# Kernel optimization log

Hardware: AMD Instinct MI355X
Metric: run time of the kernel (lower is better)

Reference implementation:

```python
import jax, jax.numpy as jnp
import numpy as np

FEATS = 1024
HEAD = 16
MLP_HIDDEN = 4096
HEAD_DIM = FEATS // HEAD
SQRT_D = float(FEATS) ** 0.5  # module scales by sqrt(feats), not sqrt(head_dim)
LN_EPS = 1e-5


def layer_norm(x, g, b):
    mu = jnp.mean(x, axis=-1, keepdims=True)
    var = jnp.mean(jnp.square(x - mu), axis=-1, keepdims=True)
    return (x - mu) * jax.lax.rsqrt(var + LN_EPS) * g + b


def setup_inputs() -> dict:
    key = jax.random.key(0)
    ks = jax.random.split(key, 12)
    s = 1.0 / np.sqrt(FEATS)
    s2 = 1.0 / np.sqrt(MLP_HIDDEN)
    return {
        "x": jax.random.normal(ks[0], (2, 2048, FEATS), dtype=jnp.float32),
        "ln1_g": jnp.ones((FEATS,), jnp.float32),
        "ln1_b": jnp.zeros((FEATS,), jnp.float32),
        "wq": jax.random.normal(ks[1], (FEATS, FEATS), jnp.float32) * s,
        "bq": jnp.zeros((FEATS,), jnp.float32),
        "wk": jax.random.normal(ks[2], (FEATS, FEATS), jnp.float32) * s,
        "bk": jnp.zeros((FEATS,), jnp.float32),
        "wv": jax.random.normal(ks[3], (FEATS, FEATS), jnp.float32) * s,
        "bv": jnp.zeros((FEATS,), jnp.float32),
        "wo": jax.random.normal(ks[4], (FEATS, FEATS), jnp.float32) * s,
        "bo": jnp.zeros((FEATS,), jnp.float32),
        "ln2_g": jnp.ones((FEATS,), jnp.float32),
        "ln2_b": jnp.zeros((FEATS,), jnp.float32),
        "w1": jax.random.normal(ks[5], (MLP_HIDDEN, FEATS), jnp.float32) * s,
        "b1": jnp.zeros((MLP_HIDDEN,), jnp.float32),
        "w2": jax.random.normal(ks[6], (FEATS, MLP_HIDDEN), jnp.float32) * s2,
        "b2": jnp.zeros((FEATS,), jnp.float32),
    }


def reference(x, ln1_g, ln1_b, wq, bq, wk, bk, wv, bv, wo, bo,
              ln2_g, ln2_b, w1, b1, w2, b2):
    b, n, f = x.shape
    h = layer_norm(x, ln1_g, ln1_b)
    # qkv projections (torch Linear: y = x @ W.T + b)
    q = (h @ wq.T + bq).reshape(b, n, HEAD, HEAD_DIM).transpose(0, 2, 1, 3)
    k = (h @ wk.T + bk).reshape(b, n, HEAD, HEAD_DIM).transpose(0, 2, 1, 3)
    v = (h @ wv.T + bv).reshape(b, n, HEAD, HEAD_DIM).transpose(0, 2, 1, 3)
    score = jax.nn.softmax(jnp.einsum('bhif,bhjf->bhij', q, k) / SQRT_D, axis=-1)
    attn = jnp.einsum('bhij,bhjf->bihf', score, v).reshape(b, n, f)
    o = attn @ wo.T + bo
    out1 = o + x
    h2 = layer_norm(out1, ln2_g, ln2_b)
    mlp = jax.nn.relu(jax.nn.relu(h2 @ w1.T + b1) @ w2.T + b2)
    return mlp + out1
```

## Files before the change

kernel.cpp:

```cpp
#include <hip/hip_runtime.h>
#include <hip/hip_bf16.h>

#define FEATS 1024
#define NH 16
#define HD 64
#define SEQ 2048
#define BATCH 2
#define MTOT (BATCH*SEQ)
#define MLPH 4096
#define QSCALE 0.04508422277369218f

typedef __attribute__((ext_vector_type(8))) short bf16x8;
typedef __attribute__((ext_vector_type(4))) short bf16x4;
typedef __attribute__((ext_vector_type(4))) float f32x4;

static_assert(sizeof(bf16x8) == 16, "bf16x8 must be 16B");

__device__ __forceinline__ unsigned short f2bf(float f) {
    unsigned int u = __float_as_uint(f);
    unsigned int lsb = (u >> 16) & 1u;
    u += 0x7fffu + lsb;
    return (unsigned short)(u >> 16);
}

#define ASYNC16(GP, LP) __builtin_amdgcn_global_load_lds( \
    (const __attribute__((address_space(1))) void*)(GP),  \
    (__attribute__((address_space(3))) void*)(LP), 16, 0, 0)

__global__ __launch_bounds__(256) void cvt_all_kernel(
    const float* __restrict__ wq, const float* __restrict__ wk,
    const float* __restrict__ wv, const float* __restrict__ wo,
    const float* __restrict__ w1, const float* __restrict__ w2,
    unsigned short* __restrict__ dst) {
    const size_t i = ((size_t)blockIdx.x * 256 + threadIdx.x) * 4;
    const size_t MB = (size_t)1024 * 1024;
    const float* s;
    size_t off;
    float sc = 1.0f;
    if (i < MB)            { s = wq; off = i;          sc = QSCALE; }
    else if (i < 2 * MB)   { s = wk; off = i - MB; }
    else if (i < 3 * MB)   { s = wv; off = i - 2 * MB; }
    else if (i < 4 * MB)   { s = wo; off = i - 3 * MB; }
    else if (i < 8 * MB)   { s = w1; off = i - 4 * MB; }
    else                   { s = w2; off = i - 8 * MB; }
    float4 v = *(const float4*)(s + off);
    ushort4 o;
    o.x = f2bf(v.x * sc); o.y = f2bf(v.y * sc);
    o.z = f2bf(v.z * sc); o.w = f2bf(v.w * sc);
    *(ushort4*)(dst + i) = o;
}

__global__ __launch_bounds__(256) void concat3_kernel(const float* __restrict__ a,
                                                      const float* __restrict__ b,
                                                      const float* __restrict__ c,
                                                      float* __restrict__ o) {
    int i = blockIdx.x * 256 + threadIdx.x;
    float v = (i < 1024) ? a[i] * QSCALE : ((i < 2048) ? b[i - 1024] : c[i - 2048]);
    o[i] = v;
}

__global__ __launch_bounds__(256) void ln_kernel(const float* __restrict__ x,
                                                 const float* __restrict__ g,
                                                 const float* __restrict__ bta,
                                                 unsigned short* __restrict__ h) {
    __shared__ float red[8];
    const int row = blockIdx.x;
    const int t = threadIdx.x;
    const float* xr = x + (size_t)row * FEATS;
    float4 v = ((const float4*)xr)[t];
    float s  = v.x + v.y + v.z + v.w;
    float ss = v.x * v.x + v.y * v.y + v.z * v.z + v.w * v.w;
#pragma unroll
    for (int off = 1; off < 64; off <<= 1) {
        s  += __shfl_xor(s, off);
        ss += __shfl_xor(ss, off);
    }
    const int w = t >> 6;
    if ((t & 63) == 0) { red[w] = s; red[4 + w] = ss; }
    __syncthreads();
    s  = red[0] + red[1] + red[2] + red[3];
    ss = red[4] + red[5] + red[6] + red[7];
    const float mu  = s * (1.f / FEATS);
    const float var = ss * (1.f / FEATS) - mu * mu;
    const float rs  = rsqrtf(var + 1e-5f);
    float4 gv = ((const float4*)g)[t];
    float4 bv = ((const float4*)bta)[t];
    ushort4 ov;
    ov.x = f2bf((v.x - mu) * rs * gv.x + bv.x);
    ov.y = f2bf((v.y - mu) * rs * gv.y + bv.y);
    ov.z = f2bf((v.z - mu) * rs * gv.z + bv.z);
    ov.w = f2bf((v.w - mu) * rs * gv.w + bv.w);
    ((ushort4*)h)[(size_t)row * (FEATS / 4) + t] = ov;
}

template <bool RELU, bool ADD, bool OUTBF16>
__global__ __launch_bounds__(256, 3)
void gemm_kernel(const unsigned short* __restrict__ A,
                 const unsigned short* __restrict__ W,
                 const float* __restrict__ bias,
                 const float* __restrict__ addend,
                 void* __restrict__ outp,
                 int M, int N, int K, int gx) {
    __shared__ unsigned short lds[3][2][128 * 32];

    const int t = threadIdx.x;
    const int w = t >> 6, lane = t & 63;
    const int wr = w >> 1, wc = w & 1;
    const int li = lane & 15, lj = lane >> 4;

    const int nwg = gridDim.x;
    const int cpx = nwg >> 3;
    const int wg = blockIdx.x;
    const int swz = (wg & 7) * cpx + (wg >> 3);
    const int mb = (swz / gx) * 128, nb = (swz % gx) * 128;

    const int srow = lane >> 2;
    const int scg = ((lane & 3) ^ (srow & 3)) * 8;
    const unsigned short* gA = A + (size_t)(mb + w * 16 + srow) * K + scg;
    const unsigned short* gB = W + (size_t)(nb + w * 16 + srow) * K + scg;
    const size_t half = (size_t)64 * K;
    const int lbase = w * 512 + lane * 8;

    const int rsw = (lj ^ (li & 3)) * 8;

    const int nt = K >> 5;

#define STAGE(BUF, K0)                                             \
    do {                                                           \
        unsigned short* la_ = &lds[BUF][0][lbase];                 \
        unsigned short* lb_ = &lds[BUF][1][lbase];                 \
        ASYNC16(gA + (K0), la_);                                   \
        ASYNC16(gA + half + (K0), la_ + 2048);                     \
        ASYNC16(gB + (K0), lb_);                                   \
        ASYNC16(gB + half + (K0), lb_ + 2048);                     \
    } while (0)

    STAGE(0, 0);
    STAGE(1, 32);
    asm volatile("s_waitcnt vmcnt(4)" ::: "memory");
    __builtin_amdgcn_s_barrier();

    f32x4 acc[4][4] = {};

    for (int i = 0; i < nt; ++i) {
        const int cur = i % 3;
        const unsigned short* Al = &lds[cur][0][0];
        const unsigned short* Bl = &lds[cur][1][0];

        bf16x8 af[4], bfr[4];
#pragma unroll
        for (int m = 0; m < 4; m++)
            af[m] = *(const bf16x8*)(Al + (wr * 64 + m * 16 + li) * 32 + rsw);
#pragma unroll
        for (int n = 0; n < 4; n++)
            bfr[n] = *(const bf16x8*)(Bl + (wc * 64 + n * 16 + li) * 32 + rsw);

        const int pf = i + 2 < nt;
        if (pf) STAGE((i + 2) % 3, (i + 2) * 32);

#pragma unroll
        for (int m = 0; m < 4; m++)
#pragma unroll
            for (int n = 0; n < 4; n++)
                acc[m][n] = __builtin_amdgcn_mfma_f32_16x16x32_bf16(af[m], bfr[n], acc[m][n], 0, 0, 0);

        if (i + 1 < nt) {
            if (pf) asm volatile("s_waitcnt vmcnt(4)" ::: "memory");
            else    asm volatile("s_waitcnt vmcnt(0)" ::: "memory");
            __builtin_amdgcn_s_barrier();
        }
    }
#undef STAGE

#pragma unroll
    for (int m = 0; m < 4; m++) {
#pragma unroll
        for (int n = 0; n < 4; n++) {
            const int col = nb + wc * 64 + n * 16 + li;
            const float bv = bias[col];
#pragma unroll
            for (int r = 0; r < 4; r++) {
                const int row = mb + wr * 64 + m * 16 + lj * 4 + r;
                float v = acc[m][n][r] + bv;
                if (RELU) v = fmaxf(v, 0.f);
                if (ADD)  v += addend[(size_t)row * N + col];
                if (OUTBF16)
                    ((unsigned short*)outp)[(size_t)row * N + col] = f2bf(v);
                else
                    ((float*)outp)[(size_t)row * N + col] = v;
            }
        }
    }
}

__global__ __launch_bounds__(256) void vtrans_kernel(const unsigned short* __restrict__ qkv,
                                                     unsigned short* __restrict__ vt) {
    constexpr int LDV = 68;
    __shared__ unsigned short Vl[64 * LDV];
    const int bh = blockIdx.x, st = blockIdx.y;
    const int b = bh >> 4, h = bh & 15;
    const int t = threadIdx.x;
    const unsigned short* src = qkv + (size_t)(b * SEQ + st * 64) * (3 * FEATS) + 2 * FEATS + h * HD;
#pragma unroll
    for (int i = 0; i < 2; i++) {
        int idx = t + i * 256;
        int r = idx >> 3, c = (idx & 7) * 8;
        *(bf16x8*)(Vl + r * LDV + c) = *(const bf16x8*)(src + (size_t)r * (3 * FEATS) + c);
    }
    __syncthreads();
    unsigned short* dst = vt + (size_t)bh * HD * SEQ + st * 64;
#pragma unroll
    for (int i = 0; i < 2; i++) {
        int idx = t + i * 256;
        int d = idx >> 3, s8 = (idx & 7) * 8;
        const int base = s8 & ~31;
        const int u4 = ((s8 >> 3) & 3) * 4;
        bf16x8 v;
#pragma unroll
        for (int j = 0; j < 8; j++) {
            const int key = base + u4 + (j & 3) + ((j >> 2) & 1) * 16;
            v[j] = Vl[key * LDV + d];
        }
        *(bf16x8*)(dst + (size_t)d * SEQ + s8) = v;
    }
}

__global__ __launch_bounds__(256, 4)
void attn_kernel(const unsigned short* __restrict__ qkv,
                 const unsigned short* __restrict__ vt,
                 unsigned short* __restrict__ out) {
    constexpr int LK = 72;
    __shared__ unsigned short Kl[2][64 * LK];
    __shared__ unsigned short Vtl[2][64 * LK];

    const int bh = blockIdx.x;
    const int b = bh >> 4, h = bh & 15;
    const int q0 = blockIdx.y * 128;
    const int t = threadIdx.x, w = t >> 6, lane = t & 63;
    const int li = lane & 15, lj = lane >> 4;

    const size_t rstr = 3 * FEATS;
    const unsigned short* qkvb = qkv + (size_t)(b * SEQ) * rstr;
    const unsigned short* ksrc = qkvb + FEATS + h * HD;
    const unsigned short* vsrc = vt + (size_t)bh * HD * SEQ;

    bf16x8 aq[2][2];
#pragma unroll
    for (int hh = 0; hh < 2; hh++)
#pragma unroll
        for (int kk = 0; kk < 2; kk++)
            aq[hh][kk] = *(const bf16x8*)(qkvb +
                (size_t)(q0 + w * 32 + hh * 16 + li) * rstr + h * HD + kk * 32 + lj * 8);

    f32x4 o[2][4] = {};
    f32x4 oS[2] = {};

    const short onebf = (short)0x3F80;
    const bf16x8 ones = {onebf, onebf, onebf, onebf, onebf, onebf, onebf, onebf};

    const int sr = t >> 2, sc = (t & 3) * 16;
    const unsigned short* kg = ksrc + (size_t)sr * rstr + sc;
    const unsigned short* vg = vsrc + (size_t)sr * SEQ + sc;
    const int ldo = sr * LK + sc;

    const int nt = SEQ / 64;

    {
        bf16x8 k0 = *(const bf16x8*)kg;
        bf16x8 k1 = *(const bf16x8*)(kg + 8);
        bf16x8 v0 = *(const bf16x8*)vg;
        bf16x8 v1 = *(const bf16x8*)(vg + 8);
        *(bf16x8*)(&Kl[0][ldo])      = k0;
        *(bf16x8*)(&Kl[0][ldo + 8])  = k1;
        *(bf16x8*)(&Vtl[0][ldo])     = v0;
        *(bf16x8*)(&Vtl[0][ldo + 8]) = v1;
    }

    int cur = 0;
    for (int i = 0; i < nt; ++i) {
        bf16x8 kr0, kr1, vr0, vr1;
        if (i + 1 < nt) {
            const unsigned short* kn = kg + (size_t)(i + 1) * 64 * rstr;
            const unsigned short* vn = vg + (i + 1) * 64;
            kr0 = *(const bf16x8*)kn;
            kr1 = *(const bf16x8*)(kn + 8);
            vr0 = *(const bf16x8*)vn;
            vr1 = *(const bf16x8*)(vn + 8);
        }

        asm volatile("s_waitcnt lgkmcnt(0)" ::: "memory");
        __builtin_amdgcn_s_barrier();

        const unsigned short* Kc = Kl[cur];
        const unsigned short* Vc = Vtl[cur];

        f32x4 s[2][4];
        __builtin_amdgcn_s_setprio(1);
#pragma unroll
        for (int n = 0; n < 4; n++) {
            bf16x8 k0 = *(const bf16x8*)(Kc + (n * 16 + li) * LK + lj * 8);
            bf16x8 k1 = *(const bf16x8*)(Kc + (n * 16 + li) * LK + 32 + lj * 8);
#pragma unroll
            for (int hh = 0; hh < 2; hh++) {
                f32x4 acc = {};
                acc = __builtin_amdgcn_mfma_f32_16x16x32_bf16(k0, aq[hh][0], acc, 0, 0, 0);
                acc = __builtin_amdgcn_mfma_f32_16x16x32_bf16(k1, aq[hh][1], acc, 0, 0, 0);
                s[hh][n] = acc;
            }
        }
        __builtin_amdgcn_s_setprio(0);

        bf16x8 A[2][2];
#pragma unroll
        for (int hh = 0; hh < 2; hh++)
#pragma unroll
            for (int kk = 0; kk < 2; kk++) {
                float p[8];
#pragma unroll
                for (int r = 0; r < 4; r++) {
                    p[r]     = exp2f(s[hh][2 * kk][r]);
                    p[4 + r] = exp2f(s[hh][2 * kk + 1][r]);
                }
                union { unsigned u[4]; bf16x8 v; } Au;
                asm("v_cvt_pk_bf16_f32 %0, %1, %2" : "=v"(Au.u[0]) : "v"(p[0]), "v"(p[1]));
                asm("v_cvt_pk_bf16_f32 %0, %1, %2" : "=v"(Au.u[1]) : "v"(p[2]), "v"(p[3]));
                asm("v_cvt_pk_bf16_f32 %0, %1, %2" : "=v"(Au.u[2]) : "v"(p[4]), "v"(p[5]));
                asm("v_cvt_pk_bf16_f32 %0, %1, %2" : "=v"(Au.u[3]) : "v"(p[6]), "v"(p[7]));
                A[hh][kk] = Au.v;
            }

#pragma unroll
        for (int hh = 0; hh < 2; hh++)
#pragma unroll
            for (int kk = 0; kk < 2; kk++)
                oS[hh] = __builtin_amdgcn_mfma_f32_16x16x32_bf16(A[hh][kk], ones, oS[hh], 0, 0, 0);

        __builtin_amdgcn_s_setprio(1);
#pragma unroll
        for (int n = 0; n < 4; n++) {
#pragma unroll
            for (int kk = 0; kk < 2; kk++) {
                bf16x8 bv = *(const bf16x8*)(Vc + (n * 16 + li) * LK + kk * 32 + lj * 8);
                o[0][n] = __builtin_amdgcn_mfma_f32_16x16x32_bf16(A[0][kk], bv, o[0][n], 0, 0, 0);
                o[1][n] = __builtin_amdgcn_mfma_f32_16x16x32_bf16(A[1][kk], bv, o[1][n], 0, 0, 0);
            }
        }
        __builtin_amdgcn_s_setprio(0);

        if (i + 1 < nt) {
            *(bf16x8*)(&Kl[cur ^ 1][ldo])      = kr0;
            *(bf16x8*)(&Kl[cur ^ 1][ldo + 8])  = kr1;
            *(bf16x8*)(&Vtl[cur ^ 1][ldo])     = vr0;
            *(bf16x8*)(&Vtl[cur ^ 1][ldo + 8]) = vr1;
        }
        cur ^= 1;
    }

    unsigned short* ob = out + (size_t)(b * SEQ + q0 + w * 32) * FEATS + h * HD;
#pragma unroll
    for (int hh = 0; hh < 2; hh++)
#pragma unroll
        for (int r = 0; r < 4; r++) {
            const float inv = 1.f / oS[hh][r];
#pragma unroll
            for (int n = 0; n < 4; n++)
                ob[(size_t)(hh * 16 + lj * 4 + r) * FEATS + n * 16 + li] =
                    f2bf(o[hh][n][r] * inv);
        }
}

extern "C" void kernel_launch(void* const* d_in, const int* in_sizes, int n_in,
                              void* d_out, int out_size, void* d_ws, size_t ws_size,
                              hipStream_t stream) {
    const float* x     = (const float*)d_in[0];
    const float* ln1_g = (const float*)d_in[1];
    const float* ln1_b = (const float*)d_in[2];
    const float* wq    = (const float*)d_in[3];
    const float* bq    = (const float*)d_in[4];
    const float* wk    = (const float*)d_in[5];
    const float* bk    = (const float*)d_in[6];
    const float* wv    = (const float*)d_in[7];
    const float* bvv   = (const float*)d_in[8];
    const float* wo    = (const float*)d_in[9];
    const float* bo    = (const float*)d_in[10];
    const float* ln2_g = (const float*)d_in[11];
    const float* ln2_b = (const float*)d_in[12];
    const float* w1    = (const float*)d_in[13];
    const float* b1    = (const float*)d_in[14];
    const float* w2    = (const float*)d_in[15];
    const float* b2    = (const float*)d_in[16];

    unsigned short* wqkv_b = (unsigned short*)d_ws;
    unsigned short* wo_b   = wqkv_b + 3072 * 1024;
    unsigned short* w1_b   = wo_b + 1024 * 1024;
    unsigned short* w2_b   = w1_b + 4096 * 1024;
    float*          bqkv   = (float*)(w2_b + 1024 * 4096);
    unsigned short* region = (unsigned short*)(bqkv + 3072);
    unsigned short* qkvb   = region;
    unsigned short* hb     = region + (size_t)4096 * 3072;
    unsigned short* vtb    = hb;
    unsigned short* a1     = region;
    unsigned short* attn_o = region + (size_t)4096 * 4096;
    unsigned short* h2     = attn_o;
    float*          out1   = (float*)(attn_o + (size_t)4096 * 1024);
    float*          outf   = (float*)d_out;

    dim3 blk(256);

    cvt_all_kernel<<<12288, blk, 0, stream>>>(wq, wk, wv, wo, w1, w2, wqkv_b);
    concat3_kernel<<<12, blk, 0, stream>>>(bq, bk, bvv, bqkv);

    ln_kernel<<<MTOT, blk, 0, stream>>>(x, ln1_g, ln1_b, hb);

    gemm_kernel<false, false, true><<<768, blk, 0, stream>>>(
        hb, wqkv_b, bqkv, nullptr, qkvb, MTOT, 3072, FEATS, 24);

    vtrans_kernel<<<dim3(BATCH * NH, SEQ / 64), blk, 0, stream>>>(qkvb, vtb);

    attn_kernel<<<dim3(BATCH * NH, SEQ / 128), dim3(256), 0, stream>>>(qkvb, vtb, attn_o);

    gemm_kernel<false, true, false><<<256, blk, 0, stream>>>(
        attn_o, wo_b, bo, x, out1, MTOT, FEATS, FEATS, 8);

    ln_kernel<<<MTOT, blk, 0, stream>>>(out1, ln2_g, ln2_b, h2);

    gemm_kernel<true, false, true><<<1024, blk, 0, stream>>>(
        h2, w1_b, b1, nullptr, a1, MTOT, MLPH, FEATS, 32);

    gemm_kernel<true, true, false><<<256, blk, 0, stream>>>(
        a1, w2_b, b2, out1, outf, MTOT, FEATS, MLPH, 8);
}
```

Before: 233.3 us.

## Split attention over two KV halves and combine partial results

Adds a grid z-dimension so each attention block processes half of the key sequence, writing unnormalized bf16 partial outputs and row denominators to a scratch buffer. A new combine kernel sums the two partials and normalizes. This doubles the number of attention blocks to fill more CUs, at the cost of extra global traffic, an additional launch, and rounding unnormalized partials to bf16.

```diff
diff --git a/kernel.cpp b/kernel.cpp
--- a/kernel.cpp
+++ b/kernel.cpp
@@ -228,7 +228,8 @@
 __global__ __launch_bounds__(256, 4)
 void attn_kernel(const unsigned short* __restrict__ qkv,
                  const unsigned short* __restrict__ vt,
-                 unsigned short* __restrict__ out) {
+                 unsigned short* __restrict__ nbuf,
+                 float* __restrict__ den) {
     constexpr int LK = 72;
     __shared__ unsigned short Kl[2][64 * LK];
     __shared__ unsigned short Vtl[2][64 * LK];
@@ -236,6 +237,7 @@
     const int bh = blockIdx.x;
     const int b = bh >> 4, h = bh & 15;
     const int q0 = blockIdx.y * 128;
+    const int sp = blockIdx.z;
     const int t = threadIdx.x, w = t >> 6, lane = t & 63;
     const int li = lane & 15, lj = lane >> 4;
 
@@ -259,11 +261,11 @@
     const bf16x8 ones = {onebf, onebf, onebf, onebf, onebf, onebf, onebf, onebf};
 
     const int sr = t >> 2, sc = (t & 3) * 16;
-    const unsigned short* kg = ksrc + (size_t)sr * rstr + sc;
-    const unsigned short* vg = vsrc + (size_t)sr * SEQ + sc;
+    const unsigned short* kg = ksrc + (size_t)(sp * 1024 + sr) * rstr + sc;
+    const unsigned short* vg = vsrc + (size_t)sr * SEQ + sp * 1024 + sc;
     const int ldo = sr * LK + sc;
 
-    const int nt = SEQ / 64;
+    const int nt = 1024 / 64;
 
     {
         bf16x8 k0 = *(const bf16x8*)kg;
@@ -356,17 +358,44 @@
         cur ^= 1;
     }
 
-    unsigned short* ob = out + (size_t)(b * SEQ + q0 + w * 32) * FEATS + h * HD;
+    unsigned short* ob = nbuf + (size_t)sp * MTOT * FEATS +
+                         (size_t)(b * SEQ + q0 + w * 32) * FEATS + h * HD;
 #pragma unroll
     for (int hh = 0; hh < 2; hh++)
 #pragma unroll
-        for (int r = 0; r < 4; r++) {
-            const float inv = 1.f / oS[hh][r];
+        for (int r = 0; r < 4; r++)
 #pragma unroll
             for (int n = 0; n < 4; n++)
                 ob[(size_t)(hh * 16 + lj * 4 + r) * FEATS + n * 16 + li] =
-                    f2bf(o[hh][n][r] * inv);
-        }
+                    f2bf(o[hh][n][r]);
+    if (li == 0) {
+        const int grow0 = b * SEQ + q0 + w * 32;
+#pragma unroll
+        for (int hh = 0; hh < 2; hh++)
+#pragma unroll
+            for (int r = 0; r < 4; r++)
+                den[((size_t)sp * MTOT + grow0 + hh * 16 + lj * 4 + r) * NH + h] =
+                    oS[hh][r];
+    }
+}
+
+__global__ __launch_bounds__(256) void combine_kernel(
+    const unsigned short* __restrict__ nbuf, const float* __restrict__ den,
+    unsigned short* __restrict__ out) {
+    const int row = blockIdx.x, t = threadIdx.x;
+    const int h = t >> 4;
+    const float d = den[(size_t)row * NH + h] +
+                    den[(size_t)MTOT * NH + (size_t)row * NH + h];
+    const float inv = 1.f / d;
+    const ushort4 a = *(const ushort4*)(nbuf + (size_t)row * FEATS + t * 4);
+    const ushort4 bvv = *(const ushort4*)(nbuf + (size_t)MTOT * FEATS +
+                                          (size_t)row * FEATS + t * 4);
+    ushort4 ov;
+    ov.x = f2bf((__uint_as_float((unsigned)a.x << 16) + __uint_as_float((unsigned)bvv.x << 16)) * inv);
+    ov.y = f2bf((__uint_as_float((unsigned)a.y << 16) + __uint_as_float((unsigned)bvv.y << 16)) * inv);
+    ov.z = f2bf((__uint_as_float((unsigned)a.z << 16) + __uint_as_float((unsigned)bvv.z << 16)) * inv);
+    ov.w = f2bf((__uint_as_float((unsigned)a.w << 16) + __uint_as_float((unsigned)bvv.w << 16)) * inv);
+    *(ushort4*)(out + (size_t)row * FEATS + t * 4) = ov;
 }
 
 extern "C" void kernel_launch(void* const* d_in, const int* in_sizes, int n_in,
@@ -403,6 +432,8 @@
     unsigned short* attn_o = region + (size_t)4096 * 4096;
     unsigned short* h2     = attn_o;
     float*          out1   = (float*)(attn_o + (size_t)4096 * 1024);
+    unsigned short* nbuf   = (unsigned short*)out1;
+    float*          denb   = (float*)(out1 + (size_t)4096 * 1024);
     float*          outf   = (float*)d_out;
 
     dim3 blk(256);
@@ -417,7 +448,9 @@
 
     vtrans_kernel<<<dim3(BATCH * NH, SEQ / 64), blk, 0, stream>>>(qkvb, vtb);
 
-    attn_kernel<<<dim3(BATCH * NH, SEQ / 128), dim3(256), 0, stream>>>(qkvb, vtb, attn_o);
+    attn_kernel<<<dim3(BATCH * NH, SEQ / 128, 2), dim3(256), 0, stream>>>(
+        qkvb, vtb, nbuf, denb);
+    combine_kernel<<<MTOT, blk, 0, stream>>>(nbuf, denb, attn_o);
 
     gemm_kernel<false, true, false><<<256, blk, 0, stream>>>(
         attn_o, wo_b, bo, x, out1, MTOT, FEATS, FEATS, 8);
```

New measurement: 238.5 us. +2.2%, slower.
